# Kernel optimization log

Measured on AMD Instinct MI355X. Metric: run time of the kernel, lower is better.

## Reference

```python
import jax, jax.numpy as jnp
import numpy as np


def setup_inputs() -> dict:
    key = jax.random.key(0)
    ks = jax.random.split(key, 8)
    H = 256  # hidden_size
    NH = 8   # num_heads
    HD = H // NH
    B, G = 256, 1024
    s = 1.0 / np.sqrt(H)
    return {
        "query": jax.random.normal(ks[0], (B, 2 * H), dtype=jnp.float32),
        "ref": jax.random.normal(ks[1], (B, G, H), dtype=jnp.float32),
        "Wq": jax.random.normal(ks[2], (H, 2 * H), dtype=jnp.float32) * s,
        "bq": jax.random.normal(ks[3], (H,), dtype=jnp.float32) * s,
        "We": jax.random.normal(ks[4], (H, H), dtype=jnp.float32) * s,
        "be": jax.random.normal(ks[5], (H,), dtype=jnp.float32) * s,
        "Wv": jax.random.normal(ks[6], (HD,), dtype=jnp.float32) * (1.0 / np.sqrt(HD)),
        "bv": jax.random.normal(ks[7], (1,), dtype=jnp.float32) * 0.01,
        "num_heads": 8,
    }


def reference(query, ref, Wq, bq, We, be, Wv, bv, num_heads):
    B, G, H = ref.shape
    hd = H // num_heads
    # q_dense: [B, 2H] -> [B, H] -> [B, nh, hd]
    q = (query @ Wq.T + bq).reshape(B, num_heads, hd)
    # e_dense: [B, G, H] -> [B, G, H] -> [B, G, nh, hd]
    e = (jnp.einsum('bgh,oh->bgo', ref, We) + be).reshape(B, G, num_heads, hd)
    # broadcast-add over graph dim, tanh, per-head linear scorer (hd -> 1)
    v = jnp.tanh(q[:, None, :, :] + e)                 # [B, G, nh, hd]
    s = jnp.einsum('bgnd,d->bgn', v, Wv) + bv[0]       # [B, G, nh]
    # sum over heads, output [B, 1, G] (matches sum(dim=1).transpose(1,2))
    return s.sum(axis=-1)[:, None, :]
```

## Files before the change

### kernel.cpp

```cpp
#include <hip/hip_runtime.h>

typedef __attribute__((ext_vector_type(8))) short short8;
typedef __attribute__((ext_vector_type(8))) unsigned short ushort8;
typedef __attribute__((ext_vector_type(4))) float f32x4;
typedef unsigned short ushort;
typedef unsigned int uint;

__device__ __forceinline__ ushort f2bf(float f) {
    uint x = __float_as_uint(f);
    x += 0x7fffu + ((x >> 16) & 1u);
    return (ushort)(x >> 16);
}

__global__ __launch_bounds__(256) void prep(
    const float* __restrict__ query, const float* __restrict__ Wq,
    const float* __restrict__ bq, const float* __restrict__ be,
    const float* __restrict__ We, float* __restrict__ q_ws,
    ushort* __restrict__ Web) {
    __shared__ float qrow[512];
    const int t = threadIdx.x;
    if (blockIdx.x < 64) {
        const int i = (blockIdx.x * 256 + t) * 4;
        float4 v = *(const float4*)(We + i);
        ushort4 u;
        u.x = f2bf(v.x); u.y = f2bf(v.y); u.z = f2bf(v.z); u.w = f2bf(v.w);
        *(ushort4*)(Web + i) = u;
        return;
    }
    const int b = blockIdx.x - 64;
    qrow[t]       = query[b * 512 + t];
    qrow[t + 256] = query[b * 512 + 256 + t];
    __syncthreads();
    const f32x4* wr = (const f32x4*)(Wq + (size_t)t * 512);
    float s0 = 0.f, s1 = 0.f, s2 = 0.f, s3 = 0.f;
#pragma unroll 4
    for (int j = 0; j < 128; j += 4) {
        f32x4 w0 = wr[j], w1 = wr[j + 1], w2 = wr[j + 2], w3 = wr[j + 3];
        f32x4 q0 = *(const f32x4*)(qrow + 4 * j);
        f32x4 q1 = *(const f32x4*)(qrow + 4 * j + 4);
        f32x4 q2 = *(const f32x4*)(qrow + 4 * j + 8);
        f32x4 q3 = *(const f32x4*)(qrow + 4 * j + 12);
        s0 += w0.x * q0.x + w0.y * q0.y + w0.z * q0.z + w0.w * q0.w;
        s1 += w1.x * q1.x + w1.y * q1.y + w1.z * q1.z + w1.w * q1.w;
        s2 += w2.x * q2.x + w2.y * q2.y + w2.z * q2.z + w2.w * q2.w;
        s3 += w3.x * q3.x + w3.y * q3.y + w3.z * q3.z + w3.w * q3.w;
    }
    q_ws[b * 256 + t] = (s0 + s1) + (s2 + s3) + bq[t] + be[t];
}

#define BM 64
#define LDA 264

__global__ __launch_bounds__(256, 4) void fused_gemm(
    const float* __restrict__ ref, const ushort* __restrict__ Web,
    const float* __restrict__ q_ws, const float* __restrict__ Wv,
    const float* __restrict__ bv, float* __restrict__ out) {
    __shared__ ushort Asm[BM * LDA];
    __shared__ float red[4][64];

    const int t = threadIdx.x;
    const int w = t >> 6;
    const int l = t & 63;
    const int quad = l >> 4;
    const int lr = l & 15;
    const size_t row0 = (size_t)blockIdx.x * BM;
    const int b = (int)(row0 >> 10);

    {
        const int row = t >> 2;
        const int colbase = (t & 3) * 64;
        const float4* ap = (const float4*)(ref + (row0 + row) * 256 + colbase);
        ushort* as = Asm + row * LDA + colbase;
#pragma unroll
        for (int c = 0; c < 2; ++c) {
            float4 buf[8];
#pragma unroll
            for (int j = 0; j < 8; ++j) buf[j] = ap[c * 8 + j];
#pragma unroll
            for (int j = 0; j < 4; ++j) {
                float4 x = buf[2 * j], y = buf[2 * j + 1];
                ushort8 v;
                v[0] = f2bf(x.x); v[1] = f2bf(x.y); v[2] = f2bf(x.z); v[3] = f2bf(x.w);
                v[4] = f2bf(y.x); v[5] = f2bf(y.y); v[6] = f2bf(y.z); v[7] = f2bf(y.w);
                *(ushort8*)(as + c * 32 + j * 8) = v;
            }
        }
    }
    __syncthreads();

    f32x4 acc[4][4];
#pragma unroll
    for (int i = 0; i < 4; ++i)
#pragma unroll
        for (int j = 0; j < 4; ++j) acc[i][j] = (f32x4){0.f, 0.f, 0.f, 0.f};

    const ushort* Bp = Web + ((size_t)(w * 64 + lr)) * 256 + quad * 8;
    const ushort* Ap = Asm + lr * LDA + quad * 8;
#pragma unroll 2
    for (int k = 0; k < 8; ++k) {
        short8 bfr[4], afr[4];
#pragma unroll
        for (int cb = 0; cb < 4; ++cb)
            bfr[cb] = *(const short8*)(Bp + cb * 16 * 256 + k * 32);
#pragma unroll
        for (int rb = 0; rb < 4; ++rb)
            afr[rb] = *(const short8*)(Ap + rb * 16 * LDA + k * 32);
#pragma unroll
        for (int rb = 0; rb < 4; ++rb)
#pragma unroll
            for (int cb = 0; cb < 4; ++cb)
                acc[rb][cb] = __builtin_amdgcn_mfma_f32_16x16x32_bf16(
                    afr[rb], bfr[cb], acc[rb][cb], 0, 0, 0);
    }

    const float* qe = q_ws + b * 256;
    const float wv0 = Wv[lr];
    const float wv1 = Wv[16 + lr];
    float qv[4];
#pragma unroll
    for (int cb = 0; cb < 4; ++cb) qv[cb] = qe[w * 64 + cb * 16 + lr];

    float part[4][4];
#pragma unroll
    for (int rb = 0; rb < 4; ++rb)
#pragma unroll
        for (int r = 0; r < 4; ++r) part[rb][r] = 0.f;

#pragma unroll
    for (int cb = 0; cb < 4; ++cb) {
        const float wvv = (cb & 1) ? wv1 : wv0;
#pragma unroll
        for (int rb = 0; rb < 4; ++rb)
#pragma unroll
            for (int r = 0; r < 4; ++r) {
                float x = acc[rb][cb][r] + qv[cb];
                float th = 1.f - 2.f / (__expf(2.f * x) + 1.f);
                part[rb][r] += th * wvv;
            }
    }
#pragma unroll
    for (int off = 1; off < 16; off <<= 1)
#pragma unroll
        for (int rb = 0; rb < 4; ++rb)
#pragma unroll
            for (int r = 0; r < 4; ++r)
                part[rb][r] += __shfl_xor(part[rb][r], off, 64);

    if (lr == 0) {
#pragma unroll
        for (int rb = 0; rb < 4; ++rb)
#pragma unroll
            for (int r = 0; r < 4; ++r)
                red[w][rb * 16 + quad * 4 + r] = part[rb][r];
    }
    __syncthreads();
    if (t < 64) {
        float s = red[0][t] + red[1][t] + red[2][t] + red[3][t] + 8.f * bv[0];
        out[row0 + t] = s;
    }
}

extern "C" void kernel_launch(void* const* d_in, const int* in_sizes, int n_in,
                              void* d_out, int out_size, void* d_ws, size_t ws_size,
                              hipStream_t stream) {
    const float* query = (const float*)d_in[0];
    const float* ref   = (const float*)d_in[1];
    const float* Wq    = (const float*)d_in[2];
    const float* bq    = (const float*)d_in[3];
    const float* We    = (const float*)d_in[4];
    const float* be    = (const float*)d_in[5];
    const float* Wv    = (const float*)d_in[6];
    const float* bv    = (const float*)d_in[7];
    float* out = (float*)d_out;

    float*  q_ws = (float*)d_ws;
    ushort* Web  = (ushort*)((char*)d_ws + 65536 * sizeof(float));

    prep<<<320, 256, 0, stream>>>(query, Wq, bq, be, We, q_ws, Web);
    fused_gemm<<<4096, 256, 0, stream>>>(ref, Web, q_ws, Wv, bv, out);
}
```

Measured before the change: 441.8 us.

## Prefetch B fragments across k-steps and use cheaper bf16 packing

Issues the first B-fragment global loads before the A-tile staging and software-pipelines the rest, loading the next k-step's B fragments while MFMAs run on the current ones. The epilogue operands (q, Wv, bv) are also loaded before the barrier. The float-to-bf16 conversion switches from round-to-nearest-even to a round-half-up add plus byte permute, which packs two values per instruction. Launch bounds drop from 4 to 3 waves per SIMD to give room for the extra registers, at the cost of occupancy and slightly different rounding.

Result: no change. 444.1 us (+0.5%).

```diff
diff --git a/kernel.cpp b/kernel.cpp
--- a/kernel.cpp
+++ b/kernel.cpp
@@ -10,6 +10,12 @@
     uint x = __float_as_uint(f);
     x += 0x7fffu + ((x >> 16) & 1u);
     return (ushort)(x >> 16);
+}
+
+__device__ __forceinline__ uint pack2bf(float x, float y) {
+    uint xi = __float_as_uint(x) + 0x8000u;
+    uint yi = __float_as_uint(y) + 0x8000u;
+    return __builtin_amdgcn_perm(yi, xi, 0x07060302u);
 }
 
 __global__ __launch_bounds__(256) void prep(
@@ -51,7 +57,7 @@
 #define BM 64
 #define LDA 264
 
-__global__ __launch_bounds__(256, 4) void fused_gemm(
+__global__ __launch_bounds__(256, 3) void fused_gemm(
     const float* __restrict__ ref, const ushort* __restrict__ Web,
     const float* __restrict__ q_ws, const float* __restrict__ Wv,
     const float* __restrict__ bv, float* __restrict__ out) {
@@ -66,11 +72,17 @@
     const size_t row0 = (size_t)blockIdx.x * BM;
     const int b = (int)(row0 >> 10);
 
+    const ushort* Bp = Web + ((size_t)(w * 64 + lr)) * 256 + quad * 8;
+    short8 bcur[4];
+#pragma unroll
+    for (int cb = 0; cb < 4; ++cb)
+        bcur[cb] = *(const short8*)(Bp + cb * 16 * 256);
+
     {
         const int row = t >> 2;
         const int colbase = (t & 3) * 64;
         const float4* ap = (const float4*)(ref + (row0 + row) * 256 + colbase);
-        ushort* as = Asm + row * LDA + colbase;
+        uint* as = (uint*)(Asm + row * LDA + colbase);
 #pragma unroll
         for (int c = 0; c < 2; ++c) {
             float4 buf[8];
@@ -79,46 +91,56 @@
 #pragma unroll
             for (int j = 0; j < 4; ++j) {
                 float4 x = buf[2 * j], y = buf[2 * j + 1];
-                ushort8 v;
-                v[0] = f2bf(x.x); v[1] = f2bf(x.y); v[2] = f2bf(x.z); v[3] = f2bf(x.w);
-                v[4] = f2bf(y.x); v[5] = f2bf(y.y); v[6] = f2bf(y.z); v[7] = f2bf(y.w);
-                *(ushort8*)(as + c * 32 + j * 8) = v;
+                uint4 p;
+                p.x = pack2bf(x.x, x.y);
+                p.y = pack2bf(x.z, x.w);
+                p.z = pack2bf(y.x, y.y);
+                p.w = pack2bf(y.z, y.w);
+                *(uint4*)(as + c * 16 + j * 4) = p;
             }
         }
-    }
-    __syncthreads();
-
-    f32x4 acc[4][4];
-#pragma unroll
-    for (int i = 0; i < 4; ++i)
-#pragma unroll
-        for (int j = 0; j < 4; ++j) acc[i][j] = (f32x4){0.f, 0.f, 0.f, 0.f};
-
-    const ushort* Bp = Web + ((size_t)(w * 64 + lr)) * 256 + quad * 8;
-    const ushort* Ap = Asm + lr * LDA + quad * 8;
-#pragma unroll 2
-    for (int k = 0; k < 8; ++k) {
-        short8 bfr[4], afr[4];
-#pragma unroll
-        for (int cb = 0; cb < 4; ++cb)
-            bfr[cb] = *(const short8*)(Bp + cb * 16 * 256 + k * 32);
-#pragma unroll
-        for (int rb = 0; rb < 4; ++rb)
-            afr[rb] = *(const short8*)(Ap + rb * 16 * LDA + k * 32);
-#pragma unroll
-        for (int rb = 0; rb < 4; ++rb)
-#pragma unroll
-            for (int cb = 0; cb < 4; ++cb)
-                acc[rb][cb] = __builtin_amdgcn_mfma_f32_16x16x32_bf16(
-                    afr[rb], bfr[cb], acc[rb][cb], 0, 0, 0);
     }
 
     const float* qe = q_ws + b * 256;
     const float wv0 = Wv[lr];
     const float wv1 = Wv[16 + lr];
+    const float bvv = bv[0];
     float qv[4];
 #pragma unroll
     for (int cb = 0; cb < 4; ++cb) qv[cb] = qe[w * 64 + cb * 16 + lr];
+
+    __syncthreads();
+
+    f32x4 acc[4][4];
+#pragma unroll
+    for (int i = 0; i < 4; ++i)
+#pragma unroll
+        for (int j = 0; j < 4; ++j) acc[i][j] = (f32x4){0.f, 0.f, 0.f, 0.f};
+
+    const ushort* Ap = Asm + lr * LDA + quad * 8;
+#pragma unroll
+    for (int k = 0; k < 8; ++k) {
+        short8 bnxt[4];
+        if (k < 7) {
+#pragma unroll
+            for (int cb = 0; cb < 4; ++cb)
+                bnxt[cb] = *(const short8*)(Bp + cb * 16 * 256 + (k + 1) * 32);
+        }
+        short8 afr[4];
+#pragma unroll
+        for (int rb = 0; rb < 4; ++rb)
+            afr[rb] = *(const short8*)(Ap + rb * 16 * LDA + k * 32);
+#pragma unroll
+        for (int rb = 0; rb < 4; ++rb)
+#pragma unroll
+            for (int cb = 0; cb < 4; ++cb)
+                acc[rb][cb] = __builtin_amdgcn_mfma_f32_16x16x32_bf16(
+                    afr[rb], bcur[cb], acc[rb][cb], 0, 0, 0);
+        if (k < 7) {
+#pragma unroll
+            for (int cb = 0; cb < 4; ++cb) bcur[cb] = bnxt[cb];
+        }
+    }
 
     float part[4][4];
 #pragma unroll
@@ -155,7 +177,7 @@
     }
     __syncthreads();
     if (t < 64) {
-        float s = red[0][t] + red[1][t] + red[2][t] + red[3][t] + 8.f * bv[0];
+        float s = red[0][t] + red[1][t] + red[2][t] + red[3][t] + 8.f * bvv;
         out[row0 + t] = s;
     }
 }
```
